# Kernel optimization log

Hardware: AMD Instinct MI355X
Metric: run time of the kernel (lower is better)

Reference implementation:

```python
import math
import jax, jax.numpy as jnp
import numpy as np

B, DIM, H = 16, 1024, 16
HD = DIM // H                      # 64
P_ORIG = 1024                      # num_patches arg
NP = math.ceil(math.sqrt(P_ORIG)) ** 2 // 2   # 512 attended tokens
ALPHA, BETA, GAMMA = 1.9, 3.8, 15.2           # iRPE euc config, ratio=1.9
NUM_BUCKETS = 2 * int(BETA) + 1               # 7


def _rp_bucket(L):
    """Static euclidean-distance relative-position buckets (iRPE 'euc')."""
    E = int(math.ceil(math.sqrt(L)))
    flat = np.arange(E * E)
    pos = np.stack([flat // E, flat % E], axis=1)[:L].astype(np.float64)  # [L,2]
    diff = pos[:, None, :] - pos[None, :, :]
    dis = np.round(np.sqrt((diff ** 2).sum(-1)))
    far = np.round(ALPHA + np.log(np.maximum(dis, 1e-9) / ALPHA)
                   / math.log(GAMMA / ALPHA) * (BETA - ALPHA))
    idx = np.where(dis <= ALPHA, np.round(dis), np.minimum(far, BETA)).astype(np.int32)
    idx = idx - idx.min()
    return jnp.asarray(idx)  # [L,L] int32 in [0, int(BETA)]

RP_BUCKET = _rp_bucket(NP)


def setup_inputs() -> dict:
    key = jax.random.key(0)
    ks = jax.random.split(key, 7)
    s = 0.02
    return {
        "x": jax.random.normal(ks[0], (B, P_ORIG, DIM), dtype=jnp.float32),
        "wq": jax.random.normal(ks[1], (DIM, DIM), dtype=jnp.float32) * s,
        "wk": jax.random.normal(ks[2], (DIM, DIM), dtype=jnp.float32) * s,
        "wv": jax.random.normal(ks[3], (DIM, DIM), dtype=jnp.float32) * s,
        "rpe_w": jax.random.normal(ks[4], (HD, NUM_BUCKETS), dtype=jnp.float32) * s,
        "proj_w": jax.random.normal(ks[5], (DIM, DIM), dtype=jnp.float32) * s,
        "proj_b": jax.random.normal(ks[6], (DIM,), dtype=jnp.float32) * s,
    }


def reference(x, wq, wk, wv, rpe_w, proj_w, proj_b):
    # F.pad on token axis with pad = NP - N (negative => crop)
    pad = NP - x.shape[1]
    if pad >= 0:
        x = jnp.pad(x, ((0, 0), (0, pad), (0, 0)))
    else:
        x = x[:, :NP, :]
    b = x.shape[0]
    scale = HD ** (-0.5)

    def heads(t):  # [b,NP,DIM] -> [b,H,NP,HD]
        return t.reshape(b, NP, H, HD).transpose(0, 2, 1, 3)

    q = heads(x @ wq.T)
    k = heads(x @ wk.T)
    v = heads(x @ wv.T)

    attn = jnp.einsum('bhid,bhjd->bhij', q, k) * scale
    # contextual RPE on keys (transposed): bias[b,h,i,j] = q[b,h,i,:] . W[:, bucket[i,j]]
    lt = jnp.einsum('bhid,dn->bhin', q, rpe_w)                 # [b,H,NP,NB]
    bias = jnp.take_along_axis(lt, RP_BUCKET[None, None, :, :], axis=3)  # [b,H,NP,NP]
    attn = jax.nn.softmax(attn + bias, axis=-1)

    out = jnp.einsum('bhij,bhjd->bhid', attn, v)
    out = out.transpose(0, 2, 1, 3).reshape(b, NP, DIM)
    out = out @ proj_w.T + proj_b
    return out[:, :P_ORIG, :]
```

## Files before the change

kernel.cpp:

```cpp
#include <hip/hip_runtime.h>

typedef __attribute__((ext_vector_type(8))) __bf16 bf16x8;
typedef __attribute__((ext_vector_type(4))) float f32x4;

#define DEVI static __device__ __forceinline__

DEVI unsigned short f2bf(float f) {
  unsigned int u = __float_as_uint(f);
  u += 0x7fffu + ((u >> 16) & 1u);
  return (unsigned short)(u >> 16);
}
DEVI float bf2f(unsigned short s) {
  return __uint_as_float(((unsigned int)s) << 16);
}

union Frag {
  bf16x8 v;
  __bf16 hf[8];
  unsigned short h[8];
  unsigned int w[4];
};

typedef __attribute__((address_space(1))) const void gv_t;
typedef __attribute__((address_space(3))) void sv_t;
#define GLOAD_LDS16(gp, lp) __builtin_amdgcn_global_load_lds((gv_t*)(gp), (sv_t*)(lp), 16, 0, 0)

#define QSCALE 0.18033688011112042f

__global__ __launch_bounds__(256) void k_prep(
    const float* __restrict__ x, const float* __restrict__ wq,
    const float* __restrict__ wk, const float* __restrict__ wv,
    const float* __restrict__ pw,
    unsigned short* __restrict__ xb, unsigned short* __restrict__ wb,
    unsigned char* __restrict__ bkt)
{
  int t = blockIdx.x * 256 + threadIdx.x;
  if (t >= 1572864) {
    int q = t - 1572864;
    int i = q >> 9, j = q & 511;
    int ir = i / 23, ic = i - ir * 23;
    int jr = j / 23, jc = j - jr * 23;
    int dy = ir - jr, dx = ic - jc;
    double dis = rint(sqrt((double)(dy * dy + dx * dx)));
    int v;
    if (dis <= 1.9) {
      v = (int)rint(dis);
    } else {
      double far = rint(1.9 + log(dis / 1.9) * (1.9 / log(8.0)));
      v = (int)fmin(far, 3.8);
    }
    bkt[q] = (unsigned char)v;
    return;
  }
  const float* src;
  unsigned short* dst;
  if (t < 1048576) {
    long e0 = (long)t << 3;
    int m = (int)(e0 >> 10), cc = (int)(e0 & 1023);
    int b = m >> 9, i = m & 511;
    src = x + (((long)(b << 10) + i) << 10) + cc;
    dst = xb + ((long)m << 10) + cc;
  } else {
    long e0 = (long)(t - 1048576) << 3;
    int mat = (int)(e0 >> 20);
    long off = e0 & 1048575;
    const float* s = (mat == 0) ? wq : (mat == 1) ? wk : (mat == 2) ? wv : pw;
    src = s + off;
    dst = wb + e0;
  }
  float4 a = *(const float4*)src;
  float4 b4 = *(const float4*)(src + 4);
  uint4 o;
  o.x = f2bf(a.x)  | ((unsigned)f2bf(a.y)  << 16);
  o.y = f2bf(a.z)  | ((unsigned)f2bf(a.w)  << 16);
  o.z = f2bf(b4.x) | ((unsigned)f2bf(b4.y) << 16);
  o.w = f2bf(b4.z) | ((unsigned)f2bf(b4.w) << 16);
  *(uint4*)dst = o;
}

__global__ __launch_bounds__(512) void k_gemm8(
    const unsigned short* __restrict__ A,
    const unsigned short* __restrict__ Bw,
    unsigned short* __restrict__ qh, unsigned short* __restrict__ kh,
    unsigned short* __restrict__ vt)
{
  __shared__ unsigned short sL[2 * 28672];

  const int bid = blockIdx.x;
  const int swz = (bid & 7) * 64 + (bid >> 3);
  const int tileN = swz & 15, tileM = swz >> 4;

  const int t = threadIdx.x;
  const int w = t >> 6, lane = t & 63;
  const int g4 = lane >> 4, c = lane & 15;
  const int wm = w >> 2, wn = w & 3;

  const char* lbase = (const char*)sL;
  const int acb = c * 64 + ((g4 * 16) ^ ((c & 8) ? 32 : 0));
  const int aoffbase = wm * 8192 + acb;
  int boff[3][2];
#pragma unroll
  for (int ni = 0; ni < 3; ++ni) {
    int row = wn * 48 + ni * 16 + c;
    int base = 32768 + (row >> 6) * 8192 + (row & 63) * 128;
    int rx = row & 7;
#pragma unroll
    for (int kk = 0; kk < 2; ++kk)
      boff[ni][kk] = base + (((kk * 4 + g4) ^ rx) << 4);
  }

  const int rowa = w * 16 + (lane >> 2);
  const int cola = ((lane & 3) * 8) ^ (((lane >> 2) & 8) ? 16 : 0);
  const unsigned short* sAp = A + (long)(tileM * 256 + rowa) * 1024 + cola;
  char* ldsta = (char*)sL + t * 16;
  const int rowbb = t >> 3;
  const int colbb = ((t & 7) ^ ((t >> 3) & 7)) * 8;
  const unsigned short* sBp = Bw + (long)(tileN * 192 + rowbb) * 1024 + colbb;
  char* ldstb = (char*)sL + 32768 + t * 16;

#define STGA(rh, kh, kn, ob) \
  GLOAD_LDS16(sAp + (long)(kn) * 64 + (rh) * 131072 + (kh) * 32, \
              ldsta + (ob) + (kh) * 16384 + (rh) * 8192)
#define STGB(gg, kn, ob) \
  GLOAD_LDS16(sBp + (long)(kn) * 64 + (gg) * 65536, \
              ldstb + (ob) + (gg) * 8192)

  f32x4 acc[8][3] = {};

  STGA(0, 0, 0, 0); STGA(1, 0, 0, 0);
  STGB(0, 0, 0); STGB(1, 0, 0); STGB(2, 0, 0);
  STGA(0, 1, 0, 0); STGA(1, 1, 0, 0);

#pragma unroll 1
  for (int kt = 0; kt < 16; ++kt) {
    const int cb = (kt & 1) ? 57344 : 0;
    const int ob = cb ^ 57344;
    const int kn = (kt < 15) ? kt + 1 : 15;

    {
      asm volatile("s_waitcnt vmcnt(2)" ::: "memory");
      __builtin_amdgcn_s_barrier();
      bf16x8 aa[4], bbf[3];
#pragma unroll
      for (int q = 0; q < 4; ++q)
        aa[q] = *(const bf16x8*)(lbase + cb + aoffbase + q * 1024);
#pragma unroll
      for (int ni = 0; ni < 3; ++ni)
        bbf[ni] = *(const bf16x8*)(lbase + cb + boff[ni][0]);
      STGA(0, 0, kn, ob); STGA(1, 0, kn, ob); STGB(0, kn, ob);
      __builtin_amdgcn_s_setprio(1);
#pragma unroll
      for (int mi = 0; mi < 4; ++mi)
#pragma unroll
        for (int ni = 0; ni < 3; ++ni)
          acc[mi][ni] = __builtin_amdgcn_mfma_f32_16x16x32_bf16(aa[mi], bbf[ni], acc[mi][ni], 0, 0, 0);
      __builtin_amdgcn_s_setprio(0);
      bf16x8 a2[4];
#pragma unroll
      for (int q = 0; q < 4; ++q)
        a2[q] = *(const bf16x8*)(lbase + cb + aoffbase + (4 + q) * 1024);
      STGB(1, kn, ob); STGB(2, kn, ob);
      __builtin_amdgcn_s_setprio(1);
#pragma unroll
      for (int mi = 0; mi < 4; ++mi)
#pragma unroll
        for (int ni = 0; ni < 3; ++ni)
          acc[4 + mi][ni] = __builtin_amdgcn_mfma_f32_16x16x32_bf16(a2[mi], bbf[ni], acc[4 + mi][ni], 0, 0, 0);
      __builtin_amdgcn_s_setprio(0);
    }
    {
      asm volatile("s_waitcnt vmcnt(5)" ::: "memory");
      __builtin_amdgcn_s_barrier();
      bf16x8 aa[4], bbf[3];
#pragma unroll
      for (int q = 0; q < 4; ++q)
        aa[q] = *(const bf16x8*)(lbase + cb + 16384 + aoffbase + q * 1024);
#pragma unroll
      for (int ni = 0; ni < 3; ++ni)
        bbf[ni] = *(const bf16x8*)(lbase + cb + boff[ni][1]);
      STGA(0, 1, kn, ob);
      __builtin_amdgcn_s_setprio(1);
#pragma unroll
      for (int mi = 0; mi < 4; ++mi)
#pragma unroll
        for (int ni = 0; ni < 3; ++ni)
          acc[mi][ni] = __builtin_amdgcn_mfma_f32_16x16x32_bf16(aa[mi], bbf[ni], acc[mi][ni], 0, 0, 0);
      __builtin_amdgcn_s_setprio(0);
      bf16x8 a2[4];
#pragma unroll
      for (int q = 0; q < 4; ++q)
        a2[q] = *(const bf16x8*)(lbase + cb + 16384 + aoffbase + (4 + q) * 1024);
      STGA(1, 1, kn, ob);
      __builtin_amdgcn_s_setprio(1);
#pragma unroll
      for (int mi = 0; mi < 4; ++mi)
#pragma unroll
        for (int ni = 0; ni < 3; ++ni)
          acc[4 + mi][ni] = __builtin_amdgcn_mfma_f32_16x16x32_bf16(a2[mi], bbf[ni], acc[4 + mi][ni], 0, 0, 0);
      __builtin_amdgcn_s_setprio(0);
    }
  }
  asm volatile("s_waitcnt vmcnt(0)" ::: "memory");
#undef STGA
#undef STGB

  const int m0 = tileM * 256 + wm * 128;
  const int n0 = tileN * 192 + wn * 48;
#pragma unroll
  for (int mi = 0; mi < 8; ++mi) {
    int mrow = m0 + mi * 16 + g4 * 4;
    int b = mrow >> 9, i = mrow & 511;
#pragma unroll
    for (int ni = 0; ni < 3; ++ni) {
      int n = n0 + ni * 16 + c;
      int mat = n >> 10;
      int cc = n & 1023;
      int h = cc >> 6, d = cc & 63;
      long bh = (long)(b * 16 + h);
      if (mat == 2) {
        unsigned int w0 = f2bf(acc[mi][ni][0]) | ((unsigned)f2bf(acc[mi][ni][1]) << 16);
        unsigned int w1 = f2bf(acc[mi][ni][2]) | ((unsigned)f2bf(acc[mi][ni][3]) << 16);
        *(uint2*)(vt + (bh * 64 + d) * 512 + i) = make_uint2(w0, w1);
      } else {
        float sc = (mat == 0) ? QSCALE : 1.0f;
        unsigned short* dst = (mat == 0 ? qh : kh) + (bh * 512 + i) * 64 + d;
#pragma unroll
        for (int r = 0; r < 4; ++r)
          dst[(long)r * 64] = f2bf(acc[mi][ni][r] * sc);
      }
    }
  }
}

__global__ __launch_bounds__(512) void k_gemm_proj(
    const unsigned short* __restrict__ A,
    const unsigned short* __restrict__ Bw,
    float* __restrict__ out, const float* __restrict__ bias)
{
  __shared__ unsigned short sL[3 * 12288];

  const int bid = blockIdx.x;
  const int swz = (bid & 7) * 32 + (bid >> 3);
  const int tileN = swz % 8, tileM = swz / 8;

  const int tid = threadIdx.x;
  const int w = tid >> 6, lane = tid & 63;
  const int g = lane >> 4, c = lane & 15;
  const int wm = w >> 1, wn = w & 1;

  const int sk = (g * 8) ^ ((c & 8) ? 16 : 0);
  int offA[4], offB[4];
#pragma unroll
  for (int i = 0; i < 4; ++i) {
    offA[i] = (wm * 4 + i) * 512 + c * 32 + sk;
    offB[i] = 8192 + (wn * 4 + i) * 512 + c * 32 + sk;
  }

  const int colb = ((lane & 3) * 8) ^ ((lane >= 32) ? 16 : 0);
  const unsigned short* gA0 = A  + ((long)(tileM * 256 + w * 32 + (lane >> 2))) * 1024 + colb;
  const unsigned short* gA1 = gA0 + 16 * 1024;
  const unsigned short* gB0 = Bw + ((long)(tileN * 128 + w * 16 + (lane >> 2))) * 1024 + colb;

#define STAGE(ktile, buf) do {                                             \
    const long ko_ = (long)(ktile) * 32;                                   \
    char* base_ = (char*)sL + (buf) * 24576;                               \
    GLOAD_LDS16(gA0 + ko_, base_ + (w * 2) * 1024 + lane * 16);            \
    GLOAD_LDS16(gA1 + ko_, base_ + (w * 2 + 1) * 1024 + lane * 16);        \
    GLOAD_LDS16(gB0 + ko_, base_ + 16384 + w * 1024 + lane * 16);          \
  } while (0)

  f32x4 acc[4][4] = {};

  STAGE(0, 0);
  STAGE(1, 1);

  int rb = 0, wbuf = 2;
  for (int t = 0; t < 32; ++t) {
    asm volatile("s_waitcnt vmcnt(3)" ::: "memory");
    __builtin_amdgcn_s_barrier();
    int kt = t + 2; if (kt > 31) kt = 31;
    STAGE(kt, wbuf);

    const unsigned short* lb = sL + rb * 12288;
    bf16x8 af[4], bf[4];
#pragma unroll
    for (int i = 0; i < 4; ++i) af[i] = *(const bf16x8*)(lb + offA[i]);
#pragma unroll
    for (int i = 0; i < 4; ++i) bf[i] = *(const bf16x8*)(lb + offB[i]);

    __builtin_amdgcn_s_setprio(1);
#pragma unroll
    for (int mi = 0; mi < 4; ++mi)
#pragma unroll
      for (int ni = 0; ni < 4; ++ni)
        acc[mi][ni] = __builtin_amdgcn_mfma_f32_16x16x32_bf16(af[mi], bf[ni], acc[mi][ni], 0, 0, 0);
    __builtin_amdgcn_s_setprio(0);
    asm volatile("s_waitcnt lgkmcnt(0)" ::: "memory");

    rb = (rb == 2) ? 0 : rb + 1;
    wbuf = (wbuf == 2) ? 0 : wbuf + 1;
  }
  asm volatile("s_waitcnt vmcnt(0)" ::: "memory");
#undef STAGE

  const int m0 = tileM * 256 + wm * 64;
  const int n0 = tileN * 128 + wn * 64;
#pragma unroll
  for (int mi = 0; mi < 4; ++mi) {
    int mrow = m0 + mi * 16 + g * 4;
#pragma unroll
    for (int ni = 0; ni < 4; ++ni) {
      int n = n0 + ni * 16 + c;
      float bv = bias[n];
#pragma unroll
      for (int r = 0; r < 4; ++r)
        out[(long)(mrow + r) * 1024 + n] = acc[mi][ni][r] + bv;
    }
  }
}

__global__ __launch_bounds__(512) void k_attn(
    const unsigned short* __restrict__ qh, const unsigned short* __restrict__ kh,
    const unsigned short* __restrict__ vt, const float* __restrict__ rpe,
    const unsigned char* __restrict__ bkt, unsigned short* __restrict__ ao)
{
  __shared__ char ring[3 * 8192];
  __shared__ float lt_lds[512 * 9];
  const int head = blockIdx.x;
  const int b = head >> 4, h = head & 15;
  const int t = threadIdx.x;
  const int w = t >> 6, lane = t & 63;
  const int g = lane >> 4, c = lane & 15;
  const int qbase = w * 64;
  const unsigned short* Q = qh + (long)head * 512 * 64;
  const unsigned short* K = kh + (long)head * 512 * 64;
  const unsigned short* V = vt + (long)head * 64 * 512;

  const unsigned short* sgp;
  char* sld;
  int sjstep;
  if (t < 256) {
    int row = t >> 3;
    int chunk = (t & 7) ^ (row & 7);
    sgp = K + (long)row * 64 + chunk * 8;
    sld = ring + t * 16;
    sjstep = 64;
  } else {
    int u = t - 256;
    int row = u >> 2;
    int chunk = (u & 3) ^ (row & 3);
    sgp = V + (long)row * 512 + chunk * 8;
    sld = ring + 4096 + u * 16;
    sjstep = 1;
  }

#define STAGE(jt_, slot_) \
  GLOAD_LDS16(sgp + (long)(jt_) * 32 * sjstep, sld + (slot_) * 8192)

  Frag qu[4][2];
#pragma unroll
  for (int it = 0; it < 4; ++it)
#pragma unroll
    for (int kk = 0; kk < 2; ++kk)
      qu[it][kk].v = *(const bf16x8*)(Q + (qbase + it * 16 + c) * 64 + kk * 32 + g * 8);

  STAGE(0, 0);
  STAGE(1, 1);

  float lt[4][7] = {};
#pragma unroll
  for (int kk = 0; kk < 2; ++kk)
#pragma unroll
    for (int tt = 0; tt < 8; ++tt) {
      int d = kk * 32 + g * 8 + tt;
      const float* rr = rpe + d * 7;
      float r0 = rr[0], r1 = rr[1], r2 = rr[2], r3 = rr[3], r4 = rr[4], r5 = rr[5], r6 = rr[6];
#pragma unroll
      for (int it = 0; it < 4; ++it) {
        float qv = bf2f(qu[it][kk].h[tt]);
        lt[it][0] += qv * r0; lt[it][1] += qv * r1; lt[it][2] += qv * r2;
        lt[it][3] += qv * r3; lt[it][4] += qv * r4; lt[it][5] += qv * r5;
        lt[it][6] += qv * r6;
      }
    }
#pragma unroll
  for (int it = 0; it < 4; ++it)
#pragma unroll
    for (int n = 0; n < 7; ++n) {
      float v = lt[it][n];
      v += __shfl_xor(v, 16);
      v += __shfl_xor(v, 32);
      if (g == 0) lt_lds[(qbase + it * 16 + c) * 9 + n] = v * 8.0f;
    }

  int rowb36[4];
  const unsigned char* bktp[4];
#pragma unroll
  for (int it = 0; it < 4; ++it) {
    int row = qbase + it * 16 + c;
    rowb36[it] = row * 36;
    bktp[it] = bkt + (long)row * 512 + g * 8;
  }

  const int jperm = (c >> 2) * 8 + (c & 3);
  int koff[2][2];
#pragma unroll
  for (int jt = 0; jt < 2; ++jt) {
    int jp = jperm + jt * 4;
#pragma unroll
    for (int kk = 0; kk < 2; ++kk)
      koff[jt][kk] = jp * 128 + (((kk * 4 + g) ^ (jp & 7)) << 4);
  }
  int voff[4];
#pragma unroll
  for (int dt = 0; dt < 4; ++dt) {
    int r = dt * 16 + c;
    voff[dt] = 4096 + r * 64 + ((g ^ (r & 3)) << 4);
  }

  f32x4 oacc[4][4] = {};
  float lp[4] = {0.f, 0.f, 0.f, 0.f};

  int rb = 0, wbuf = 2;
#pragma unroll 1
  for (int kt = 0; kt < 16; ++kt) {
    asm volatile("s_waitcnt vmcnt(1)" ::: "memory");
    __builtin_amdgcn_s_barrier();
    int kn = (kt < 14) ? kt + 2 : 15;
    STAGE(kn, wbuf);

    const char* lb = ring + rb * 8192;
    const int jb = kt * 32;

    Frag kf[2][2];
#pragma unroll
    for (int jt = 0; jt < 2; ++jt)
#pragma unroll
      for (int kk = 0; kk < 2; ++kk)
        kf[jt][kk].v = *(const bf16x8*)(lb + koff[jt][kk]);

    uint2 bb[4];
#pragma unroll
    for (int it = 0; it < 4; ++it)
      bb[it] = *(const uint2*)(bktp[it] + jb);

    f32x4 s[2][4];
#pragma unroll
    for (int jt = 0; jt < 2; ++jt)
#pragma unroll
      for (int it = 0; it < 4; ++it) {
        f32x4 z = {0.f, 0.f, 0.f, 0.f};
        z = __builtin_amdgcn_mfma_f32_16x16x32_bf16(kf[jt][0].v, qu[it][0].v, z, 0, 0, 0);
        s[jt][it] = __builtin_amdgcn_mfma_f32_16x16x32_bf16(kf[jt][1].v, qu[it][1].v, z, 0, 0, 0);
      }

    Frag pfr[4];
#pragma unroll
    for (int it = 0; it < 4; ++it) {
      float ps = 0.f;
#pragma unroll
      for (int jt = 0; jt < 2; ++jt) {
        unsigned int bw = jt ? bb[it].y : bb[it].x;
#pragma unroll
        for (int r = 0; r < 4; ++r) {
          int bno = (bw >> (8 * r)) & 255;
          float bias = *(const float*)((const char*)lt_lds + rowb36[it] + (bno << 2));
          float sv = s[jt][it][r] + bias;
          float p;
          asm("v_exp_f32 %0, %1" : "=v"(p) : "v"(sv));
          ps += p;
          pfr[it].hf[jt * 4 + r] = (__bf16)p;
        }
      }
      lp[it] += ps;
    }

    bf16x8 vf[4];
#pragma unroll
    for (int dt = 0; dt < 4; ++dt)
      vf[dt] = *(const bf16x8*)(lb + voff[dt]);

#pragma unroll
    for (int dt = 0; dt < 4; ++dt)
#pragma unroll
      for (int it = 0; it < 4; ++it)
        oacc[dt][it] = __builtin_amdgcn_mfma_f32_16x16x32_bf16(vf[dt], pfr[it].v, oacc[dt][it], 0, 0, 0);

    asm volatile("s_waitcnt lgkmcnt(0)" ::: "memory");
    rb = (rb == 2) ? 0 : rb + 1;
    wbuf = (wbuf == 2) ? 0 : wbuf + 1;
  }
  asm volatile("s_waitcnt vmcnt(0)" ::: "memory");
#undef STAGE

  float li[4];
#pragma unroll
  for (int it = 0; it < 4; ++it) {
    float v = lp[it];
    v += __shfl_xor(v, 16);
    v += __shfl_xor(v, 32);
    li[it] = 1.0f / v;
  }
#pragma unroll
  for (int dt = 0; dt < 4; ++dt)
#pragma unroll
    for (int it = 0; it < 4; ++it) {
      int irow = qbase + it * 16 + c;
      int d0 = dt * 16 + g * 4;
      unsigned int w0 = f2bf(oacc[dt][it][0] * li[it]) | ((unsigned)f2bf(oacc[dt][it][1] * li[it]) << 16);
      unsigned int w1 = f2bf(oacc[dt][it][2] * li[it]) | ((unsigned)f2bf(oacc[dt][it][3] * li[it]) << 16);
      *(uint2*)(ao + ((long)(b * 512 + irow)) * 1024 + h * 64 + d0) = make_uint2(w0, w1);
    }
}

extern "C" void kernel_launch(void* const* d_in, const int* in_sizes, int n_in,
                              void* d_out, int out_size, void* d_ws, size_t ws_size,
                              hipStream_t stream) {
  const float* x   = (const float*)d_in[0];
  const float* wq  = (const float*)d_in[1];
  const float* wk  = (const float*)d_in[2];
  const float* wv  = (const float*)d_in[3];
  const float* rpe = (const float*)d_in[4];
  const float* pw  = (const float*)d_in[5];
  const float* pb  = (const float*)d_in[6];
  float* out = (float*)d_out;

  char* ws = (char*)d_ws;
  unsigned short* xb  = (unsigned short*)(ws);
  unsigned short* wb  = (unsigned short*)(ws + 16777216);
  unsigned short* qhp = (unsigned short*)(ws + 25165824);
  unsigned short* khp = (unsigned short*)(ws + 41943040);
  unsigned short* vtp = (unsigned short*)(ws + 58720256);
  unsigned char*  bkt = (unsigned char*)(ws + 75497472);
  unsigned short* aop = xb;

  k_prep<<<dim3(7168), dim3(256), 0, stream>>>(x, wq, wk, wv, pw, xb, wb, bkt);
  k_gemm8<<<dim3(512), dim3(512), 0, stream>>>(xb, wb, qhp, khp, vtp);
  k_attn<<<dim3(256), dim3(512), 0, stream>>>(qhp, khp, vtp, rpe, bkt, aop);
  k_gemm_proj<<<dim3(256), dim3(512), 0, stream>>>(aop, wb + 3 * 1048576, out, pb);
}
```

Baseline: 148.4 us.

## Split attention over two KV halves with merge kernel; re-pipeline QKV GEMM loop

The attention kernel now launches two blocks per head, each covering half of the key/value tiles. Each block writes unnormalized partial outputs and row sums, using the output buffer as scratch for the second half. A new merge kernel adds the two partials and normalizes them before the projection GEMM. The intent is to double the block count so more CUs are busy, at the cost of an extra kernel launch and added memory traffic. Separately, the QKV GEMM main loop is split into four MFMA phases with extra barriers and rearranged global-to-LDS staging, to change how loads overlap with compute.

Result: slower. 169.1 us (+14.0%).

```diff
diff --git a/kernel.cpp b/kernel.cpp
--- a/kernel.cpp
+++ b/kernel.cpp
@@ -130,6 +130,18 @@
   STGA(0, 0, 0, 0); STGA(1, 0, 0, 0);
   STGB(0, 0, 0); STGB(1, 0, 0); STGB(2, 0, 0);
   STGA(0, 1, 0, 0); STGA(1, 1, 0, 0);
+  asm volatile("s_waitcnt vmcnt(2)" ::: "memory");
+  __builtin_amdgcn_s_barrier();
+
+#define MFMA12(base_, AREG, BREG)                                           \
+  do {                                                                      \
+    _Pragma("unroll")                                                       \
+    for (int mi_ = 0; mi_ < 4; ++mi_)                                       \
+      _Pragma("unroll")                                                     \
+      for (int ni_ = 0; ni_ < 3; ++ni_)                                     \
+        acc[(base_) + mi_][ni_] = __builtin_amdgcn_mfma_f32_16x16x32_bf16(  \
+            AREG[mi_], BREG[ni_], acc[(base_) + mi_][ni_], 0, 0, 0);        \
+  } while (0)
 
 #pragma unroll 1
   for (int kt = 0; kt < 16; ++kt) {
@@ -137,70 +149,55 @@
     const int ob = cb ^ 57344;
     const int kn = (kt < 15) ? kt + 1 : 15;
 
-    {
-      asm volatile("s_waitcnt vmcnt(2)" ::: "memory");
-      __builtin_amdgcn_s_barrier();
-      bf16x8 aa[4], bbf[3];
-#pragma unroll
-      for (int q = 0; q < 4; ++q)
-        aa[q] = *(const bf16x8*)(lbase + cb + aoffbase + q * 1024);
-#pragma unroll
-      for (int ni = 0; ni < 3; ++ni)
-        bbf[ni] = *(const bf16x8*)(lbase + cb + boff[ni][0]);
-      STGA(0, 0, kn, ob); STGA(1, 0, kn, ob); STGB(0, kn, ob);
-      __builtin_amdgcn_s_setprio(1);
-#pragma unroll
-      for (int mi = 0; mi < 4; ++mi)
-#pragma unroll
-        for (int ni = 0; ni < 3; ++ni)
-          acc[mi][ni] = __builtin_amdgcn_mfma_f32_16x16x32_bf16(aa[mi], bbf[ni], acc[mi][ni], 0, 0, 0);
-      __builtin_amdgcn_s_setprio(0);
-      bf16x8 a2[4];
-#pragma unroll
-      for (int q = 0; q < 4; ++q)
-        a2[q] = *(const bf16x8*)(lbase + cb + aoffbase + (4 + q) * 1024);
-      STGB(1, kn, ob); STGB(2, kn, ob);
-      __builtin_amdgcn_s_setprio(1);
-#pragma unroll
-      for (int mi = 0; mi < 4; ++mi)
-#pragma unroll
-        for (int ni = 0; ni < 3; ++ni)
-          acc[4 + mi][ni] = __builtin_amdgcn_mfma_f32_16x16x32_bf16(a2[mi], bbf[ni], acc[4 + mi][ni], 0, 0, 0);
-      __builtin_amdgcn_s_setprio(0);
-    }
-    {
-      asm volatile("s_waitcnt vmcnt(5)" ::: "memory");
-      __builtin_amdgcn_s_barrier();
-      bf16x8 aa[4], bbf[3];
-#pragma unroll
-      for (int q = 0; q < 4; ++q)
-        aa[q] = *(const bf16x8*)(lbase + cb + 16384 + aoffbase + q * 1024);
-#pragma unroll
-      for (int ni = 0; ni < 3; ++ni)
-        bbf[ni] = *(const bf16x8*)(lbase + cb + boff[ni][1]);
-      STGA(0, 1, kn, ob);
-      __builtin_amdgcn_s_setprio(1);
-#pragma unroll
-      for (int mi = 0; mi < 4; ++mi)
-#pragma unroll
-        for (int ni = 0; ni < 3; ++ni)
-          acc[mi][ni] = __builtin_amdgcn_mfma_f32_16x16x32_bf16(aa[mi], bbf[ni], acc[mi][ni], 0, 0, 0);
-      __builtin_amdgcn_s_setprio(0);
-      bf16x8 a2[4];
-#pragma unroll
-      for (int q = 0; q < 4; ++q)
-        a2[q] = *(const bf16x8*)(lbase + cb + 16384 + aoffbase + (4 + q) * 1024);
-      STGA(1, 1, kn, ob);
-      __builtin_amdgcn_s_setprio(1);
-#pragma unroll
-      for (int mi = 0; mi < 4; ++mi)
-#pragma unroll
-        for (int ni = 0; ni < 3; ++ni)
-          acc[4 + mi][ni] = __builtin_amdgcn_mfma_f32_16x16x32_bf16(a2[mi], bbf[ni], acc[4 + mi][ni], 0, 0, 0);
-      __builtin_amdgcn_s_setprio(0);
-    }
+    bf16x8 aa[4], bbf[3];
+#pragma unroll
+    for (int q = 0; q < 4; ++q) aa[q] = *(const bf16x8*)(lbase + cb + aoffbase + q * 1024);
+#pragma unroll
+    for (int ni = 0; ni < 3; ++ni) bbf[ni] = *(const bf16x8*)(lbase + cb + boff[ni][0]);
+    STGA(0, 0, kn, ob); STGA(1, 0, kn, ob);
+    __builtin_amdgcn_s_barrier();
+    asm volatile("s_waitcnt lgkmcnt(0)" ::: "memory");
+    __builtin_amdgcn_s_setprio(1);
+    MFMA12(0, aa, bbf);
+    __builtin_amdgcn_s_setprio(0);
+    __builtin_amdgcn_s_barrier();
+
+#pragma unroll
+    for (int q = 0; q < 4; ++q) aa[q] = *(const bf16x8*)(lbase + cb + aoffbase + (4 + q) * 1024);
+    STGB(0, kn, ob); STGB(1, kn, ob);
+    __builtin_amdgcn_s_barrier();
+    asm volatile("s_waitcnt lgkmcnt(0)" ::: "memory");
+    __builtin_amdgcn_s_setprio(1);
+    MFMA12(4, aa, bbf);
+    __builtin_amdgcn_s_setprio(0);
+    asm volatile("s_waitcnt vmcnt(4)" ::: "memory");
+    __builtin_amdgcn_s_barrier();
+
+#pragma unroll
+    for (int q = 0; q < 4; ++q) aa[q] = *(const bf16x8*)(lbase + cb + 16384 + aoffbase + q * 1024);
+#pragma unroll
+    for (int ni = 0; ni < 3; ++ni) bbf[ni] = *(const bf16x8*)(lbase + cb + boff[ni][1]);
+    STGB(2, kn, ob); STGA(0, 1, kn, ob);
+    __builtin_amdgcn_s_barrier();
+    asm volatile("s_waitcnt lgkmcnt(0)" ::: "memory");
+    __builtin_amdgcn_s_setprio(1);
+    MFMA12(0, aa, bbf);
+    __builtin_amdgcn_s_setprio(0);
+    __builtin_amdgcn_s_barrier();
+
+#pragma unroll
+    for (int q = 0; q < 4; ++q) aa[q] = *(const bf16x8*)(lbase + cb + 16384 + aoffbase + (4 + q) * 1024);
+    STGA(1, 1, kn, ob);
+    __builtin_amdgcn_s_barrier();
+    asm volatile("s_waitcnt lgkmcnt(0)" ::: "memory");
+    __builtin_amdgcn_s_setprio(1);
+    MFMA12(4, aa, bbf);
+    __builtin_amdgcn_s_setprio(0);
+    asm volatile("s_waitcnt vmcnt(2)" ::: "memory");
+    __builtin_amdgcn_s_barrier();
   }
   asm volatile("s_waitcnt vmcnt(0)" ::: "memory");
+#undef MFMA12
 #undef STGA
 #undef STGB
 
@@ -322,19 +319,25 @@
 __global__ __launch_bounds__(512) void k_attn(
     const unsigned short* __restrict__ qh, const unsigned short* __restrict__ kh,
     const unsigned short* __restrict__ vt, const float* __restrict__ rpe,
-    const unsigned char* __restrict__ bkt, unsigned short* __restrict__ ao)
+    const unsigned char* __restrict__ bkt,
+    unsigned short* __restrict__ po0, unsigned short* __restrict__ po1,
+    float* __restrict__ ls0, float* __restrict__ ls1)
 {
   __shared__ char ring[3 * 8192];
   __shared__ float lt_lds[512 * 9];
-  const int head = blockIdx.x;
+  const int bid = blockIdx.x;
+  const int head = bid >> 1, kvh = bid & 1;
   const int b = head >> 4, h = head & 15;
   const int t = threadIdx.x;
   const int w = t >> 6, lane = t & 63;
   const int g = lane >> 4, c = lane & 15;
   const int qbase = w * 64;
+  const int tb0 = kvh * 8;
   const unsigned short* Q = qh + (long)head * 512 * 64;
   const unsigned short* K = kh + (long)head * 512 * 64;
   const unsigned short* V = vt + (long)head * 64 * 512;
+  unsigned short* po = kvh ? po1 : po0;
+  float* lsp = kvh ? ls1 : ls0;
 
   const unsigned short* sgp;
   char* sld;
@@ -364,8 +367,8 @@
     for (int kk = 0; kk < 2; ++kk)
       qu[it][kk].v = *(const bf16x8*)(Q + (qbase + it * 16 + c) * 64 + kk * 32 + g * 8);
 
-  STAGE(0, 0);
-  STAGE(1, 1);
+  STAGE(tb0 + 0, 0);
+  STAGE(tb0 + 1, 1);
 
   float lt[4][7] = {};
 #pragma unroll
@@ -423,14 +426,14 @@
 
   int rb = 0, wbuf = 2;
 #pragma unroll 1
-  for (int kt = 0; kt < 16; ++kt) {
+  for (int kt = 0; kt < 8; ++kt) {
     asm volatile("s_waitcnt vmcnt(1)" ::: "memory");
     __builtin_amdgcn_s_barrier();
-    int kn = (kt < 14) ? kt + 2 : 15;
+    int kn = tb0 + ((kt < 6) ? kt + 2 : 7);
     STAGE(kn, wbuf);
 
     const char* lb = ring + rb * 8192;
-    const int jb = kt * 32;
+    const int jb = (tb0 + kt) * 32;
 
     Frag kf[2][2];
 #pragma unroll
@@ -493,24 +496,58 @@
   asm volatile("s_waitcnt vmcnt(0)" ::: "memory");
 #undef STAGE
 
-  float li[4];
 #pragma unroll
   for (int it = 0; it < 4; ++it) {
     float v = lp[it];
     v += __shfl_xor(v, 16);
     v += __shfl_xor(v, 32);
-    li[it] = 1.0f / v;
-  }
+    if (g == 0) lsp[head * 512 + qbase + it * 16 + c] = v;
+  }
+
 #pragma unroll
   for (int dt = 0; dt < 4; ++dt)
 #pragma unroll
     for (int it = 0; it < 4; ++it) {
       int irow = qbase + it * 16 + c;
       int d0 = dt * 16 + g * 4;
-      unsigned int w0 = f2bf(oacc[dt][it][0] * li[it]) | ((unsigned)f2bf(oacc[dt][it][1] * li[it]) << 16);
-      unsigned int w1 = f2bf(oacc[dt][it][2] * li[it]) | ((unsigned)f2bf(oacc[dt][it][3] * li[it]) << 16);
-      *(uint2*)(ao + ((long)(b * 512 + irow)) * 1024 + h * 64 + d0) = make_uint2(w0, w1);
-    }
+      unsigned int w0 = f2bf(oacc[dt][it][0]) | ((unsigned)f2bf(oacc[dt][it][1]) << 16);
+      unsigned int w1 = f2bf(oacc[dt][it][2]) | ((unsigned)f2bf(oacc[dt][it][3]) << 16);
+      *(uint2*)(po + ((long)(b * 512 + irow)) * 1024 + h * 64 + d0) = make_uint2(w0, w1);
+    }
+}
+
+__global__ __launch_bounds__(256) void k_merge(
+    const unsigned short* __restrict__ po1, const float* __restrict__ ls0,
+    const float* __restrict__ ls1, unsigned short* __restrict__ ao)
+{
+  int idx = blockIdx.x * 256 + threadIdx.x;
+  int m = idx >> 7;
+  int n0 = (idx & 127) << 3;
+  int head = (m >> 9) * 16 + (n0 >> 6);
+  int i = m & 511;
+  float li = 1.0f / (ls0[head * 512 + i] + ls1[head * 512 + i]);
+  long off = (long)m * 1024 + n0;
+  uint2 a = *(const uint2*)(ao + off);
+  uint2 bq = *(const uint2*)(po1 + off);
+  unsigned int r[2];
+#pragma unroll
+  for (int q = 0; q < 2; ++q) {
+    unsigned int ua = q ? a.y : a.x, ub = q ? bq.y : bq.x;
+    float f0 = (bf2f((unsigned short)(ua & 0xffff)) + bf2f((unsigned short)(ub & 0xffff))) * li;
+    float f1 = (bf2f((unsigned short)(ua >> 16)) + bf2f((unsigned short)(ub >> 16))) * li;
+    r[q] = f2bf(f0) | ((unsigned)f2bf(f1) << 16);
+  }
+  uint2 a2 = *(const uint2*)(ao + off + 4);
+  uint2 b2 = *(const uint2*)(po1 + off + 4);
+  unsigned int r2[2];
+#pragma unroll
+  for (int q = 0; q < 2; ++q) {
+    unsigned int ua = q ? a2.y : a2.x, ub = q ? b2.y : b2.x;
+    float f0 = (bf2f((unsigned short)(ua & 0xffff)) + bf2f((unsigned short)(ub & 0xffff))) * li;
+    float f1 = (bf2f((unsigned short)(ua >> 16)) + bf2f((unsigned short)(ub >> 16))) * li;
+    r2[q] = f2bf(f0) | ((unsigned)f2bf(f1) << 16);
+  }
+  *(uint4*)(ao + off) = make_uint4(r[0], r[1], r2[0], r2[1]);
 }
 
 extern "C" void kernel_launch(void* const* d_in, const int* in_sizes, int n_in,
@@ -532,10 +569,14 @@
   unsigned short* khp = (unsigned short*)(ws + 41943040);
   unsigned short* vtp = (unsigned short*)(ws + 58720256);
   unsigned char*  bkt = (unsigned char*)(ws + 75497472);
-  unsigned short* aop = xb;
+  unsigned short* po0 = xb;
+  unsigned short* po1 = (unsigned short*)d_out;
+  float* ls0 = (float*)((char*)d_out + 16777216);
+  float* ls1 = (float*)((char*)d_out + 17825792);
 
   k_prep<<<dim3(7168), dim3(256), 0, stream>>>(x, wq, wk, wv, pw, xb, wb, bkt);
   k_gemm8<<<dim3(512), dim3(512), 0, stream>>>(xb, wb, qhp, khp, vtp);
-  k_attn<<<dim3(256), dim3(512), 0, stream>>>(qhp, khp, vtp, rpe, bkt, aop);
-  k_gemm_proj<<<dim3(256), dim3(512), 0, stream>>>(aop, wb + 3 * 1048576, out, pb);
-}
+  k_attn<<<dim3(512), dim3(512), 0, stream>>>(qhp, khp, vtp, rpe, bkt, po0, po1, ls0, ls1);
+  k_merge<<<dim3(4096), dim3(256), 0, stream>>>(po1, ls0, ls1, po0);
+  k_gemm_proj<<<dim3(256), dim3(512), 0, stream>>>(po0, wb + 3 * 1048576, out, pb);
+}
```
